# Optimization experiments

Measured on AMD Instinct MI355X. Metric: run time of the kernel, lower is better.

The kernel has to match this reference:

```python
import jax, jax.numpy as jnp
import numpy as np
from jax import lax

NC = 80          # len(model.names)
MAX_DET = 300    # args.max_det
TOPK = 1500      # max_det * 5 candidate prune (static-shape stand-in for conf mask)
CONF = 0.25      # args.conf
IOU_TH = 0.45    # args.iou
IMGSZ = 640.0    # max(x.shape[2:])
B, A = 32, 8400  # batch, anchors for 640x640 YOLOv8


def setup_inputs() -> dict:
    key = jax.random.key(0)
    kb, kw, ks = jax.random.split(key, 3)
    # realistic xyxy boxes inside a 640x640 image
    x1y1 = jax.random.uniform(kb, (B, A, 2), dtype=jnp.float32) * 600.0
    wh = 5.0 + jax.random.uniform(kw, (B, A, 2), dtype=jnp.float32) * 35.0
    boxes = jnp.concatenate([x1y1, x1y1 + wh], axis=-1)          # [B, A, 4]
    cls_scores = jax.random.uniform(ks, (B, A, NC), dtype=jnp.float32)
    pred = jnp.concatenate([boxes, cls_scores], axis=-1)          # [B, A, 4+NC]
    return {"pred": pred.transpose(0, 2, 1)}                      # [B, 4+NC, A]


def box_iou(a, b):
    # a: [K,4] xyxy, b: [K,4] xyxy -> [K,K]
    lt = jnp.maximum(a[:, None, :2], b[None, :, :2])
    rb = jnp.minimum(a[:, None, 2:], b[None, :, 2:])
    inter = jnp.prod(jnp.clip(rb - lt, 0.0), axis=-1)
    area_a = jnp.prod(a[:, 2:] - a[:, :2], axis=-1)
    area_b = jnp.prod(b[:, 2:] - b[:, :2], axis=-1)
    return inter / (area_a[:, None] + area_b[None, :] - inter + 1e-7)


def _nms_image(boxes, scores, classes):
    # boxes [A,4], scores [A], classes [A] (int)
    valid = scores > CONF                       # score > args.conf mask
    msc = jnp.where(valid, scores, -1.0)
    _, idx = lax.top_k(msc, TOPK)               # score-desc candidate prune
    box = boxes[idx]
    cls = classes[idx]
    score = scores[idx]
    valid = valid[idx]
    # normalize + per-class offset trick (agnostic_nms=False, end=4, multiplier=1/nc)
    mult = 1.0 / NC
    nmsbox = box * (mult / IMGSZ)
    nmsbox = nmsbox + (cls.astype(box.dtype) * mult)[:, None]
    iou = box_iou(nmsbox, nmsbox)               # [TOPK, TOPK]
    ar = jnp.arange(TOPK)

    def step(i, supp):
        # greedy NMS: box i survives if not suppressed by an earlier kept box
        keep_i = jnp.logical_not(supp[i]) & valid[i]
        return supp | (keep_i & (iou[i] > IOU_TH) & (ar > i))

    supp = lax.fori_loop(0, TOPK, step, jnp.zeros((TOPK,), dtype=bool))
    keep = jnp.logical_not(supp) & valid
    # stable sort: kept boxes first (already score-ordered), take max_det, zero-pad rest
    order = jnp.argsort(jnp.where(keep, 0, 1).astype(jnp.int32))
    sel = order[:MAX_DET]
    m = keep[sel].astype(box.dtype)[:, None]
    dets = jnp.concatenate(
        [box[sel], score[sel][:, None], cls[sel].astype(box.dtype)[:, None]], axis=-1
    )                                            # [MAX_DET, 6]
    return dets * m


def reference(pred):
    # pred: [B, 4+NC, A]
    p = pred.transpose(0, 2, 1)                  # [B, A, 4+NC]
    boxes = p[..., :4]
    cls_scores = p[..., 4:4 + NC]
    scores = cls_scores.max(axis=-1)             # scores, classes = scores.max(dim=-1)
    classes = jnp.argmax(cls_scores, axis=-1)
    return jax.vmap(_nms_image)(boxes, scores, classes)  # [B, MAX_DET, 6]
```

## Files before the change

### kernel.cpp

```cpp
#include <hip/hip_runtime.h>
#include <stdint.h>

typedef unsigned long long u64;
typedef unsigned int u32;

#define NCLS 80
#define NA   8400
#define NIMG 32
#define TOPK 1500
#define MAXDET 300
#define NW 24
#define NBLK 24
#define ROWPAD (NBLK * 64)
#define CONF 0.25f
#define IOU_TH 0.45f

#define CHUNK 2048
#define NCH   5
#define CAND  1500

#define OFF_CAND   ((size_t)0)
#define OFF_TBOX   (OFF_CAND + (size_t)NIMG*NCH*CAND*8)
#define OFF_TNMS   (OFF_TBOX + (size_t)NIMG*TOPK*16)
#define OFF_TSC    (OFF_TNMS + (size_t)NIMG*TOPK*16)
#define OFF_TCL    (OFF_TSC  + (size_t)NIMG*TOPK*4)
#define OFF_MASK   (OFF_TCL  + (size_t)NIMG*TOPK*4)
#define WS_NEED    (OFF_MASK + (size_t)NIMG*ROWPAD*NW*8)


__global__ __launch_bounds__(1024) void k_sortchunk(const float* __restrict__ pred,
                                                    u64* __restrict__ cand) {
    __shared__ u64 s[CHUNK];
    const int tid = threadIdx.x;
    const int c = blockIdx.x;
    const int b = blockIdx.y;
    const int a0 = c * CHUNK;
    const float* pb = pred + (size_t)b * (4 + NCLS) * NA;

    for (int i = tid; i < CHUNK; i += 1024) {
        int a = a0 + i;
        u64 key = ~0ULL;
        if (a < NA) {
            float best = pb[(size_t)4 * NA + a];
            int bi = 0;
#pragma unroll 8
            for (int cc = 1; cc < NCLS; ++cc) {
                float v = pb[(size_t)(4 + cc) * NA + a];
                if (v > best) { best = v; bi = cc; }
            }
            float msc = (best > CONF) ? best : -1.0f;
            u32 u = __float_as_uint(msc);
            u = (u & 0x80000000u) ? ~u : (u | 0x80000000u);
            key = ((u64)(~u) << 32) | ((u64)(u32)a << 18) | ((u64)(u32)bi << 11);
        }
        s[i] = key;
    }
    __syncthreads();

    for (u32 k = 2; k <= CHUNK; k <<= 1) {
        for (u32 j = k >> 1; j > 0; j >>= 1) {
            int t = tid;
            int i = 2 * t - (t & (j - 1));
            u64 x = s[i], y = s[i + j];
            bool asc = (i & k) == 0;
            if ((x > y) == asc) { s[i] = y; s[i + j] = x; }
            __syncthreads();
        }
    }

    u64* cb = cand + ((size_t)b * NCH + c) * CAND;
    for (int i = tid; i < CAND; i += 1024) cb[i] = s[i];
}

__global__ __launch_bounds__(1024) void k_merge_gather(const float* __restrict__ pred,
                                                       const u64* __restrict__ cand,
                                                       float4* __restrict__ tbox,
                                                       float4* __restrict__ tnms,
                                                       float* __restrict__ tsc,
                                                       int* __restrict__ tcl) {
#pragma clang fp contract(off)
    __shared__ u64 sA[CHUNK];
    __shared__ u64 sB[CHUNK];
    const int tid = threadIdx.x;
    const int b = blockIdx.x;
    const u64* cb = cand + (size_t)b * NCH * CAND;

    for (int i = tid; i < CHUNK; i += 1024)
        sA[i] = (i < CAND) ? cb[i] : ~0ULL;

    for (int m = 1; m < NCH; ++m) {
        for (int i = tid; i < CHUNK; i += 1024)
            sB[i] = (i < CAND) ? cb[(size_t)m * CAND + i] : ~0ULL;
        __syncthreads();
        for (int i = tid; i < CHUNK; i += 1024) {
            u64 x = sA[i], y = sB[CHUNK - 1 - i];
            sA[i] = (x < y) ? x : y;
        }
        __syncthreads();
        for (u32 j = CHUNK >> 1; j > 0; j >>= 1) {
            int t = tid;
            int i = 2 * t - (t & (j - 1));
            u64 x = sA[i], y = sA[i + j];
            if (x > y) { sA[i] = y; sA[i + j] = x; }
            __syncthreads();
        }
    }

    const float* pb = pred + (size_t)b * (4 + NCLS) * NA;
    const float C1 = (float)((1.0 / 80.0) / 640.0);
    const float C2 = (float)(1.0 / 80.0);
    for (int r = tid; r < TOPK; r += 1024) {
        u64 key = sA[r];
        int a = (int)((key >> 18) & 0x3FFFu);
        int cl = (int)((key >> 11) & 0x7Fu);
        u32 ou = ~((u32)(key >> 32));
        u32 fb = (ou & 0x80000000u) ? (ou ^ 0x80000000u) : ~ou;
        float msc = __uint_as_float(fb);
        float x1 = pb[a], y1 = pb[NA + a], x2 = pb[2 * NA + a], y2 = pb[3 * NA + a];
        float off = (float)cl * C2;
        tbox[b * TOPK + r] = make_float4(x1, y1, x2, y2);
        tnms[b * TOPK + r] = make_float4(x1 * C1 + off, y1 * C1 + off,
                                         x2 * C1 + off, y2 * C1 + off);
        tsc[b * TOPK + r] = msc;
        tcl[b * TOPK + r] = cl;
    }
}

__global__ __launch_bounds__(256) void k_mask(const float4* __restrict__ tnms,
                                              u64* __restrict__ mask) {
#pragma clang fp contract(off)
    __shared__ float4 nb[768];
    const int b = blockIdx.y;
    const int idx = blockIdx.x;
    const int z = (idx < 24) ? 1 : 0;
    const int rb = (idx < 24) ? idx : (idx - 24);
    const int c0 = z * 768;
    const int tid = threadIdx.x;

    for (int i = tid; i < 768; i += 256) {
        int j = c0 + i;
        nb[i] = (j < TOPK) ? tnms[b * TOPK + j]
                           : make_float4(0.0f, 0.0f, 0.0f, 0.0f);
    }
    __syncthreads();

    const int r0 = rb * 64;
    const int r = r0 + (tid & 63);
    const int q = tid >> 6;
    float4 bi = (r < TOPK) ? tnms[b * TOPK + r]
                           : make_float4(0.0f, 0.0f, 0.0f, 0.0f);
    const float area_i = (bi.z - bi.x) * (bi.w - bi.y);

    u64* mrow = mask + ((size_t)b * ROWPAD + r) * NW;
#pragma unroll
    for (int wi = 0; wi < 3; ++wi) {
        const int w = z * 12 + q + wi * 4;
        u64 bits = 0ULL;
        if (w * 64 + 63 > r0) {
            const int jbase = (w - z * 12) * 64;
            const int j0 = w * 64;
#pragma unroll 4
            for (int l = 0; l < 64; ++l) {
                float4 bj = nb[jbase + l];
                float lx = fmaxf(bi.x, bj.x), ly = fmaxf(bi.y, bj.y);
                float rx = fminf(bi.z, bj.z), ry = fminf(bi.w, bj.w);
                float iw = fmaxf(rx - lx, 0.0f), ih = fmaxf(ry - ly, 0.0f);
                float inter = iw * ih;
                if (__ballot(inter > 0.0f)) {
                    float area_j = (bj.z - bj.x) * (bj.w - bj.y);
                    float iou = inter / (area_i + area_j - inter + 1e-7f);
                    bits |= ((iou > IOU_TH) && (j0 + l > r)) ? (1ULL << l) : 0ULL;
                }
            }
        }
        mrow[w] = bits;
        if (z == 1 && r0 >= 768)
            mrow[w - 12] = 0ULL;
    }
}

__device__ __forceinline__ void dense_block(const u64* ss, int t, u64& acc, int ml) {
    const int lane = threadIdx.x;
    u64 rword = ss[lane * NW + t];
    u64 dead = __shfl(acc, t);
    u64 kb = 0ULL;
#pragma unroll
    for (int ii = 0; ii < 64; ++ii) {
        u32 rlo = (u32)__builtin_amdgcn_readlane((int)(u32)(rword & 0xFFFFFFFFu), ii);
        u32 rhi = (u32)__builtin_amdgcn_readlane((int)(u32)(rword >> 32), ii);
        u64 row = ((u64)rhi << 32) | rlo;
        if (!((dead >> ii) & 1ULL)) { dead |= row; kb |= (1ULL << ii); }
    }
    u64 a0 = 0, a1 = 0, a2 = 0, a3 = 0;
#pragma unroll
    for (int q = 0; q < 16; ++q) {
        u64 v0 = ss[(4 * q + 0) * NW + ml];
        u64 v1 = ss[(4 * q + 1) * NW + ml];
        u64 v2 = ss[(4 * q + 2) * NW + ml];
        u64 v3 = ss[(4 * q + 3) * NW + ml];
        a0 |= ((kb >> (4 * q + 0)) & 1ULL) ? v0 : 0ULL;
        a1 |= ((kb >> (4 * q + 1)) & 1ULL) ? v1 : 0ULL;
        a2 |= ((kb >> (4 * q + 2)) & 1ULL) ? v2 : 0ULL;
        a3 |= ((kb >> (4 * q + 3)) & 1ULL) ? v3 : 0ULL;
    }
    acc |= a0 | a1 | a2 | a3;
}

__device__ __forceinline__ void step_block(uint4 (&R)[12], int t, u64& acc, int ml,
                                           const uint4* g4, u64* sbuf) {
    const int lane = threadIdx.x;
    u32 nz = 0;
#pragma unroll
    for (int i = 0; i < 12; ++i) nz |= (R[i].x | R[i].y | R[i].z | R[i].w);
    const u64 anym = __ballot(nz != 0);
    if (anym) {
        uint4* l4 = (uint4*)sbuf;
#pragma unroll
        for (int i = 0; i < 12; ++i) l4[i * 64 + lane] = R[i];
    }
    if (t + 2 < NBLK) {
#pragma unroll
        for (int i = 0; i < 12; ++i) R[i] = g4[(size_t)(t + 2) * 768 + i * 64 + lane];
    }
    if (anym) dense_block(sbuf, t, acc, ml);
}

__global__ __launch_bounds__(64) void k_scan(const u64* __restrict__ mask,
                                             const float4* __restrict__ tbox,
                                             const float* __restrict__ tsc,
                                             const int* __restrict__ tcl,
                                             float* __restrict__ out) {
    __shared__ u64 sbuf[64 * NW];
    const int b = blockIdx.x;
    const int lane = threadIdx.x;
    float* outb = out + (size_t)b * MAXDET * 6;
    for (int i = lane; i < MAXDET * 6; i += 64) outb[i] = 0.0f;
    __syncthreads();

    u64 validw = 0ULL;
    if (lane < NW) {
        const float4* t4 = (const float4*)(tsc + (size_t)b * TOPK);
#pragma unroll
        for (int q = 0; q < 16; ++q) {
            int i4 = lane * 16 + q;
            if (i4 < TOPK / 4) {
                float4 v = t4[i4];
                int base = q * 4;
                if (v.x > CONF) validw |= (1ULL << (base + 0));
                if (v.y > CONF) validw |= (1ULL << (base + 1));
                if (v.z > CONF) validw |= (1ULL << (base + 2));
                if (v.w > CONF) validw |= (1ULL << (base + 3));
            }
        }
    }
    u64 acc = (lane < NW) ? ~validw : ~0ULL;

    const u64* mbase = mask + (size_t)b * ROWPAD * NW;
    const uint4* g4 = (const uint4*)mbase;
    const int ml = (lane < NW) ? lane : 0;

    uint4 rA[12], rB[12];
#pragma unroll
    for (int i = 0; i < 12; ++i) rA[i] = g4[0 * 768 + i * 64 + lane];
#pragma unroll
    for (int i = 0; i < 12; ++i) rB[i] = g4[1 * 768 + i * 64 + lane];

    for (int tt = 0; tt < 12; ++tt) {
        step_block(rA, 2 * tt,     acc, ml, g4, sbuf);
        step_block(rB, 2 * tt + 1, acc, ml, g4, sbuf);
    }

    u64 keepw = (lane < NW) ? ~acc : 0ULL;
    int cnt = __popcll(keepw);
    int pre = cnt;
#pragma unroll
    for (int d = 1; d < 64; d <<= 1) {
        int o = __shfl_up(pre, d);
        if (lane >= d) pre += o;
    }
    int rbase = pre - cnt;
    u64 m = keepw;
    int idx = 0;
    while (m) {
        int l = __ffsll((long long)m) - 1;
        m &= m - 1;
        int r = rbase + idx; ++idx;
        if (r < MAXDET) {
            int j = lane * 64 + l;
            float4 bx = tbox[b * TOPK + j];
            float sc = tsc[b * TOPK + j];
            int c = tcl[b * TOPK + j];
            float* o6 = outb + r * 6;
            o6[0] = bx.x; o6[1] = bx.y; o6[2] = bx.z; o6[3] = bx.w;
            o6[4] = sc;   o6[5] = (float)c;
        }
    }
}

extern "C" void kernel_launch(void* const* d_in, const int* in_sizes, int n_in,
                              void* d_out, int out_size, void* d_ws, size_t ws_size,
                              hipStream_t stream) {
    const float* pred = (const float*)d_in[0];
    float* out = (float*)d_out;
    char* ws = (char*)d_ws;
    if (ws_size < WS_NEED) return;

    u64*    cand = (u64*)   (ws + OFF_CAND);
    float4* tbox = (float4*)(ws + OFF_TBOX);
    float4* tnms = (float4*)(ws + OFF_TNMS);
    float*  tsc  = (float*) (ws + OFF_TSC);
    int*    tcl  = (int*)   (ws + OFF_TCL);
    u64*    mask = (u64*)   (ws + OFF_MASK);

    k_sortchunk<<<dim3(NCH, NIMG), 1024, 0, stream>>>(pred, cand);
    k_merge_gather<<<NIMG, 1024, 0, stream>>>(pred, cand, tbox, tnms, tsc, tcl);
    k_mask<<<dim3(36, NIMG), 256, 0, stream>>>(tnms, mask);
    k_scan<<<NIMG, 64, 0, stream>>>(mask, tbox, tsc, tcl, out);
}
```

Before: 236.4 us.

## Replace serial merge with parallel rank-by-binary-search and skip empty mask blocks

Splits score computation into its own wide kernel, sorts 9 chunks of 1024 keys, and replaces the single-block-per-image bitonic merge with a fully parallel kernel that computes each key's global rank by binary search in the other sorted chunks, then scatters the gathered boxes directly. It also records a per-image bitmask of row blocks with any nonzero suppression bits in k_mask, and the scan kernel uses it to skip empty blocks instead of software-pipelining all block loads. This removes the serialized merge bottleneck, which used only 32 blocks. In exchange it adds a kernel launch and an atomic, and it drops the register prefetch overlap in the scan.

```diff
diff --git a/kernel.cpp b/kernel.cpp
--- a/kernel.cpp
+++ b/kernel.cpp
@@ -15,46 +15,50 @@
 #define CONF 0.25f
 #define IOU_TH 0.45f
 
-#define CHUNK 2048
-#define NCH   5
-#define CAND  1500
+#define CHUNK 1024
+#define NCH   9
+#define NPAD  (NCH * CHUNK)
 
 #define OFF_CAND   ((size_t)0)
-#define OFF_TBOX   (OFF_CAND + (size_t)NIMG*NCH*CAND*8)
+#define OFF_TBOX   (OFF_CAND + (size_t)NIMG*NPAD*8)
 #define OFF_TNMS   (OFF_TBOX + (size_t)NIMG*TOPK*16)
 #define OFF_TSC    (OFF_TNMS + (size_t)NIMG*TOPK*16)
 #define OFF_TCL    (OFF_TSC  + (size_t)NIMG*TOPK*4)
 #define OFF_MASK   (OFF_TCL  + (size_t)NIMG*TOPK*4)
-#define WS_NEED    (OFF_MASK + (size_t)NIMG*ROWPAD*NW*8)
-
-
-__global__ __launch_bounds__(1024) void k_sortchunk(const float* __restrict__ pred,
-                                                    u64* __restrict__ cand) {
+#define OFF_SUMM   (OFF_MASK + (size_t)NIMG*ROWPAD*NW*8)
+#define WS_NEED    (OFF_SUMM + (size_t)NIMG*4)
+
+
+__global__ __launch_bounds__(256) void k_score(const float* __restrict__ pred,
+                                               u64* __restrict__ cand,
+                                               u32* __restrict__ summary) {
+    const int a = blockIdx.x * 256 + threadIdx.x;
+    const int b = blockIdx.y;
+    if (a == 0) summary[b] = 0;
+    u64 key = ~0ULL;
+    if (a < NA) {
+        const float* pb = pred + (size_t)b * (4 + NCLS) * NA;
+        float best = pb[(size_t)4 * NA + a];
+        int bi = 0;
+#pragma unroll 8
+        for (int cc = 1; cc < NCLS; ++cc) {
+            float v = pb[(size_t)(4 + cc) * NA + a];
+            if (v > best) { best = v; bi = cc; }
+        }
+        float msc = (best > CONF) ? best : -1.0f;
+        u32 u = __float_as_uint(msc);
+        u = (u & 0x80000000u) ? ~u : (u | 0x80000000u);
+        key = ((u64)(~u) << 32) | ((u64)(u32)a << 18) | ((u64)(u32)bi << 11);
+    }
+    cand[(size_t)b * NPAD + a] = key;
+}
+
+__global__ __launch_bounds__(512) void k_sortchunk(u64* __restrict__ cand) {
     __shared__ u64 s[CHUNK];
     const int tid = threadIdx.x;
-    const int c = blockIdx.x;
-    const int b = blockIdx.y;
-    const int a0 = c * CHUNK;
-    const float* pb = pred + (size_t)b * (4 + NCLS) * NA;
-
-    for (int i = tid; i < CHUNK; i += 1024) {
-        int a = a0 + i;
-        u64 key = ~0ULL;
-        if (a < NA) {
-            float best = pb[(size_t)4 * NA + a];
-            int bi = 0;
-#pragma unroll 8
-            for (int cc = 1; cc < NCLS; ++cc) {
-                float v = pb[(size_t)(4 + cc) * NA + a];
-                if (v > best) { best = v; bi = cc; }
-            }
-            float msc = (best > CONF) ? best : -1.0f;
-            u32 u = __float_as_uint(msc);
-            u = (u & 0x80000000u) ? ~u : (u | 0x80000000u);
-            key = ((u64)(~u) << 32) | ((u64)(u32)a << 18) | ((u64)(u32)bi << 11);
-        }
-        s[i] = key;
-    }
+    u64* cb = cand + ((size_t)blockIdx.y * NCH + blockIdx.x) * CHUNK;
+    s[tid] = cb[tid];
+    s[tid + 512] = cb[tid + 512];
     __syncthreads();
 
     for (u32 k = 2; k <= CHUNK; k <<= 1) {
@@ -68,66 +72,59 @@
         }
     }
 
-    u64* cb = cand + ((size_t)b * NCH + c) * CAND;
-    for (int i = tid; i < CAND; i += 1024) cb[i] = s[i];
-}
-
-__global__ __launch_bounds__(1024) void k_merge_gather(const float* __restrict__ pred,
-                                                       const u64* __restrict__ cand,
-                                                       float4* __restrict__ tbox,
-                                                       float4* __restrict__ tnms,
-                                                       float* __restrict__ tsc,
-                                                       int* __restrict__ tcl) {
+    cb[tid] = s[tid];
+    cb[tid + 512] = s[tid + 512];
+}
+
+__global__ __launch_bounds__(256) void k_rank_gather(const float* __restrict__ pred,
+                                                     const u64* __restrict__ cand,
+                                                     float4* __restrict__ tbox,
+                                                     float4* __restrict__ tnms,
+                                                     float* __restrict__ tsc,
+                                                     int* __restrict__ tcl) {
 #pragma clang fp contract(off)
-    __shared__ u64 sA[CHUNK];
-    __shared__ u64 sB[CHUNK];
-    const int tid = threadIdx.x;
-    const int b = blockIdx.x;
-    const u64* cb = cand + (size_t)b * NCH * CAND;
-
-    for (int i = tid; i < CHUNK; i += 1024)
-        sA[i] = (i < CAND) ? cb[i] : ~0ULL;
-
-    for (int m = 1; m < NCH; ++m) {
-        for (int i = tid; i < CHUNK; i += 1024)
-            sB[i] = (i < CAND) ? cb[(size_t)m * CAND + i] : ~0ULL;
-        __syncthreads();
-        for (int i = tid; i < CHUNK; i += 1024) {
-            u64 x = sA[i], y = sB[CHUNK - 1 - i];
-            sA[i] = (x < y) ? x : y;
-        }
-        __syncthreads();
-        for (u32 j = CHUNK >> 1; j > 0; j >>= 1) {
-            int t = tid;
-            int i = 2 * t - (t & (j - 1));
-            u64 x = sA[i], y = sA[i + j];
-            if (x > y) { sA[i] = y; sA[i + j] = x; }
-            __syncthreads();
-        }
-    }
+    const int gid = blockIdx.x * 256 + threadIdx.x;
+    const int b = gid / NPAD;
+    const int e = gid - b * NPAD;
+    const int c = e >> 10;
+    const int idx = e & 1023;
+    const u64* img = cand + (size_t)b * NPAD;
+    const u64 key = img[(c << 10) + idx];
+    if (key == ~0ULL) return;
+
+    int rank = idx;
+    for (int c2 = 0; c2 < NCH; ++c2) {
+        if (c2 == c) continue;
+        const u64* base = img + (c2 << 10);
+        int pos = 0;
+#pragma unroll
+        for (int st = 512; st > 0; st >>= 1)
+            if (base[pos + st - 1] < key) pos += st;
+        rank += pos;
+    }
+    if (rank >= TOPK) return;
+
+    const int a = (int)((key >> 18) & 0x3FFFu);
+    const int cl = (int)((key >> 11) & 0x7Fu);
+    u32 ou = ~((u32)(key >> 32));
+    u32 fb = (ou & 0x80000000u) ? (ou ^ 0x80000000u) : ~ou;
+    const float msc = __uint_as_float(fb);
 
     const float* pb = pred + (size_t)b * (4 + NCLS) * NA;
     const float C1 = (float)((1.0 / 80.0) / 640.0);
     const float C2 = (float)(1.0 / 80.0);
-    for (int r = tid; r < TOPK; r += 1024) {
-        u64 key = sA[r];
-        int a = (int)((key >> 18) & 0x3FFFu);
-        int cl = (int)((key >> 11) & 0x7Fu);
-        u32 ou = ~((u32)(key >> 32));
-        u32 fb = (ou & 0x80000000u) ? (ou ^ 0x80000000u) : ~ou;
-        float msc = __uint_as_float(fb);
-        float x1 = pb[a], y1 = pb[NA + a], x2 = pb[2 * NA + a], y2 = pb[3 * NA + a];
-        float off = (float)cl * C2;
-        tbox[b * TOPK + r] = make_float4(x1, y1, x2, y2);
-        tnms[b * TOPK + r] = make_float4(x1 * C1 + off, y1 * C1 + off,
-                                         x2 * C1 + off, y2 * C1 + off);
-        tsc[b * TOPK + r] = msc;
-        tcl[b * TOPK + r] = cl;
-    }
+    float x1 = pb[a], y1 = pb[NA + a], x2 = pb[2 * NA + a], y2 = pb[3 * NA + a];
+    float off = (float)cl * C2;
+    tbox[b * TOPK + rank] = make_float4(x1, y1, x2, y2);
+    tnms[b * TOPK + rank] = make_float4(x1 * C1 + off, y1 * C1 + off,
+                                        x2 * C1 + off, y2 * C1 + off);
+    tsc[b * TOPK + rank] = msc;
+    tcl[b * TOPK + rank] = cl;
 }
 
 __global__ __launch_bounds__(256) void k_mask(const float4* __restrict__ tnms,
-                                              u64* __restrict__ mask) {
+                                              u64* __restrict__ mask,
+                                              u32* __restrict__ summary) {
 #pragma clang fp contract(off)
     __shared__ float4 nb[768];
     const int b = blockIdx.y;
@@ -152,6 +149,7 @@
     const float area_i = (bi.z - bi.x) * (bi.w - bi.y);
 
     u64* mrow = mask + ((size_t)b * ROWPAD + r) * NW;
+    u32 haveany = 0;
 #pragma unroll
     for (int wi = 0; wi < 3; ++wi) {
         const int w = z * 12 + q + wi * 4;
@@ -174,9 +172,11 @@
             }
         }
         mrow[w] = bits;
+        haveany |= (bits != 0ULL) ? 1u : 0u;
         if (z == 1 && r0 >= 768)
             mrow[w - 12] = 0ULL;
     }
+    if (haveany) atomicOr(&summary[b], 1u << rb);
 }
 
 __device__ __forceinline__ void dense_block(const u64* ss, int t, u64& acc, int ml) {
@@ -206,29 +206,11 @@
     acc |= a0 | a1 | a2 | a3;
 }
 
-__device__ __forceinline__ void step_block(uint4 (&R)[12], int t, u64& acc, int ml,
-                                           const uint4* g4, u64* sbuf) {
-    const int lane = threadIdx.x;
-    u32 nz = 0;
-#pragma unroll
-    for (int i = 0; i < 12; ++i) nz |= (R[i].x | R[i].y | R[i].z | R[i].w);
-    const u64 anym = __ballot(nz != 0);
-    if (anym) {
-        uint4* l4 = (uint4*)sbuf;
-#pragma unroll
-        for (int i = 0; i < 12; ++i) l4[i * 64 + lane] = R[i];
-    }
-    if (t + 2 < NBLK) {
-#pragma unroll
-        for (int i = 0; i < 12; ++i) R[i] = g4[(size_t)(t + 2) * 768 + i * 64 + lane];
-    }
-    if (anym) dense_block(sbuf, t, acc, ml);
-}
-
 __global__ __launch_bounds__(64) void k_scan(const u64* __restrict__ mask,
                                              const float4* __restrict__ tbox,
                                              const float* __restrict__ tsc,
                                              const int* __restrict__ tcl,
+                                             const u32* __restrict__ summary,
                                              float* __restrict__ out) {
     __shared__ u64 sbuf[64 * NW];
     const int b = blockIdx.x;
@@ -258,16 +240,17 @@
     const u64* mbase = mask + (size_t)b * ROWPAD * NW;
     const uint4* g4 = (const uint4*)mbase;
     const int ml = (lane < NW) ? lane : 0;
-
-    uint4 rA[12], rB[12];
-#pragma unroll
-    for (int i = 0; i < 12; ++i) rA[i] = g4[0 * 768 + i * 64 + lane];
-#pragma unroll
-    for (int i = 0; i < 12; ++i) rB[i] = g4[1 * 768 + i * 64 + lane];
-
-    for (int tt = 0; tt < 12; ++tt) {
-        step_block(rA, 2 * tt,     acc, ml, g4, sbuf);
-        step_block(rB, 2 * tt + 1, acc, ml, g4, sbuf);
+    const u32 summ = summary[b];
+
+    for (int t = 0; t < NBLK; ++t) {
+        if (!((summ >> t) & 1u)) continue;
+        uint4 R[12];
+#pragma unroll
+        for (int i = 0; i < 12; ++i) R[i] = g4[(size_t)t * 768 + i * 64 + lane];
+        uint4* l4 = (uint4*)sbuf;
+#pragma unroll
+        for (int i = 0; i < 12; ++i) l4[i * 64 + lane] = R[i];
+        dense_block(sbuf, t, acc, ml);
     }
 
     u64 keepw = (lane < NW) ? ~acc : 0ULL;
@@ -311,9 +294,11 @@
     float*  tsc  = (float*) (ws + OFF_TSC);
     int*    tcl  = (int*)   (ws + OFF_TCL);
     u64*    mask = (u64*)   (ws + OFF_MASK);
-
-    k_sortchunk<<<dim3(NCH, NIMG), 1024, 0, stream>>>(pred, cand);
-    k_merge_gather<<<NIMG, 1024, 0, stream>>>(pred, cand, tbox, tnms, tsc, tcl);
-    k_mask<<<dim3(36, NIMG), 256, 0, stream>>>(tnms, mask);
-    k_scan<<<NIMG, 64, 0, stream>>>(mask, tbox, tsc, tcl, out);
-}
+    u32*    summ = (u32*)   (ws + OFF_SUMM);
+
+    k_score<<<dim3(NPAD / 256, NIMG), 256, 0, stream>>>(pred, cand, summ);
+    k_sortchunk<<<dim3(NCH, NIMG), 512, 0, stream>>>(cand);
+    k_rank_gather<<<(NIMG * NPAD) / 256, 256, 0, stream>>>(pred, cand, tbox, tnms, tsc, tcl);
+    k_mask<<<dim3(36, NIMG), 256, 0, stream>>>(tnms, mask, summ);
+    k_scan<<<NIMG, 64, 0, stream>>>(mask, tbox, tsc, tcl, summ, out);
+}
```

Result: faster. 221.2 us (-6.4%).
